# Kernel optimization log

Hardware: AMD Instinct MI355X
Metric: run time of the kernel (lower is better)

Reference implementation:

```python
import jax, jax.numpy as jnp
import numpy as np

B, N, D = 8, 2048, 16   # batch, n_points, n_dim (num_df == D)
K, DM = 32, 256         # k neighbors, d_model


def setup_inputs() -> dict:
    key = jax.random.key(0)
    k0, k1, k2, k3, k4, k5 = jax.random.split(key, 6)
    x = jax.random.normal(k0, (B, N, D), jnp.float32)
    features = jax.random.uniform(k1, (B, D), jnp.float32)
    # nn.Linear(k, d_model, bias=False) weights: [out, in] = [DM, K]
    lim = 1.0 / np.sqrt(K)
    W_crd = jax.random.uniform(k2, (DM, K), jnp.float32, -lim, lim)
    W_ftr = jax.random.uniform(k3, (DM, K), jnp.float32, -lim, lim)
    pe_crd = 0.01 * jax.random.normal(k4, (1, 1, D, DM), jnp.float32)
    pe_ftr = 0.01 * jax.random.normal(k5, (1, 1, D, DM), jnp.float32)
    return {"x": x, "features": features, "W_crd": W_crd, "W_ftr": W_ftr,
            "pe_crd": pe_crd, "pe_ftr": pe_ftr, "k": K}


def _forward(x, features, W_crd, W_ftr, pe_crd, pe_ftr, k):
    b, n, d = x.shape
    # split coordinates vs features per-dimension
    fmask = features[:, None, :] > 0.1                 # [B,1,D]
    x_crd = jnp.where(fmask, 0.0, x)                   # masked_fill(features_, 0)
    x_ftr = jnp.where(fmask, x, 0.0)                   # masked_fill(~features_, 0)
    xc = jnp.concatenate([x_crd, x_ftr], axis=-1)      # [B,N,2D]
    # masked stats with attn_mask=None -> plain mean / unbiased std over points
    mean = jnp.mean(xc, axis=1, keepdims=True)
    std = jnp.std(xc, axis=1, keepdims=True, ddof=1)
    xc = jnp.clip((xc - mean) / (std + 1e-5), -10.0, 10.0)
    # pairwise L2 distances on coordinate part (torch.cdist, p=2)
    sq = jnp.sum(x_crd * x_crd, axis=-1)               # [B,N]
    d2 = sq[:, :, None] + sq[:, None, :] - 2.0 * jnp.einsum('bnd,bmd->bnm', x_crd, x_crd)
    dist = jnp.sqrt(jnp.maximum(d2, 0.0))              # [B,N,N]
    # k nearest neighbors (smallest distance, self included)
    _, idx = jax.lax.top_k(-dist, k)                   # [B,N,k]
    nb = xc[jnp.arange(b)[:, None, None], idx]         # gather neighbors [B,N,k,2D]
    local = nb - xc[:, :, None, :]                     # project_local: center frame
    xk = jnp.transpose(local, (0, 1, 3, 2))            # flatten=False -> [B,N,2D,k]
    crd, ftr = xk[:, :, :d, :], xk[:, :, d:, :]
    o_crd = (jnp.einsum('bnpk,dk->bnpd', crd, W_crd) + pe_crd).sum(axis=2)
    o_ftr = (jnp.einsum('bnpk,dk->bnpd', ftr, W_ftr) + pe_ftr).sum(axis=2)
    pe_loss = jnp.abs(pe_crd).sum() + jnp.abs(pe_ftr).sum()
    # dropout is identity in eval mode
    return o_crd + o_ftr, pe_loss


def reference(x, features, W_crd, W_ftr, pe_crd, pe_ftr, k):
    return _forward(x, features, W_crd, W_ftr, pe_crd, pe_ftr, k)
```

## Files before the change

kernel.cpp:

```cpp
#include <hip/hip_runtime.h>
#include <stdint.h>

#define B 8
#define N 2048
#define D 16
#define KNN 32
#define DM 256
#define CAP 256

__global__ __launch_bounds__(256) void knn_prep(
    const float* __restrict__ x, const float* __restrict__ features,
    const float* __restrict__ Wc, const float* __restrict__ Wf,
    const float* __restrict__ pec, const float* __restrict__ pef,
    float* __restrict__ xcrdT, float* __restrict__ sq,
    float* __restrict__ Tc, float* __restrict__ Tf,
    float* __restrict__ WcT, float* __restrict__ WfT,
    float* __restrict__ cbias, float* __restrict__ pe_loss_out)
{
    if (blockIdx.x == 64) {
        int dm = threadIdx.x;
        float cb = 0.f, al = 0.f;
#pragma unroll
        for (int p = 0; p < D; ++p)
            cb += pec[p * DM + dm] + pef[p * DM + dm];
#pragma unroll
        for (int p = 0; p < D; ++p)
            al += fabsf(pec[p * DM + dm]) + fabsf(pef[p * DM + dm]);
        cbias[dm] = cb;
#pragma unroll
        for (int k = 0; k < KNN; ++k) {
            WcT[k * DM + dm] = Wc[dm * KNN + k];
            WfT[k * DM + dm] = Wf[dm * KNN + k];
        }
        __shared__ float redf[256];
        redf[dm] = al; __syncthreads();
        for (int st = 128; st > 0; st >>= 1) {
            if (dm < st) redf[dm] += redf[dm + st];
            __syncthreads();
        }
        if (dm == 0) pe_loss_out[0] = redf[0];
        return;
    }

    int tid = threadIdx.x;
    int b = blockIdx.x >> 3;

    double ls[D], lq[D];
#pragma unroll
    for (int d = 0; d < D; ++d) { ls[d] = 0.0; lq[d] = 0.0; }
    for (int r = 0; r < 8; ++r) {
        const float* row = x + ((size_t)b * N + r * 256 + tid) * D;
#pragma unroll
        for (int d = 0; d < D; d += 4) {
            float4 v = *(const float4*)(row + d);
            double x0 = v.x, x1 = v.y, x2 = v.z, x3 = v.w;
            ls[d]   += x0; lq[d]   += x0 * x0;
            ls[d+1] += x1; lq[d+1] += x1 * x1;
            ls[d+2] += x2; lq[d+2] += x2 * x2;
            ls[d+3] += x3; lq[d+3] += x3 * x3;
        }
    }
#pragma unroll
    for (int d = 0; d < D; ++d) {
        double s = ls[d], q = lq[d];
#pragma unroll
        for (int st = 32; st >= 1; st >>= 1) {
            s += __shfl_xor(s, st, 64);
            q += __shfl_xor(q, st, 64);
        }
        ls[d] = s; lq[d] = q;
    }
    __shared__ double sred[4][2 * D];
    __shared__ float smean[32], sscale[32];
    int wave = tid >> 6, lane = tid & 63;
    if (lane == 0) {
#pragma unroll
        for (int d = 0; d < D; ++d) {
            sred[wave][d]     = ls[d];
            sred[wave][D + d] = lq[d];
        }
    }
    __syncthreads();
    if (tid < D) {
        int d = tid;
        double S = sred[0][d] + sred[1][d] + sred[2][d] + sred[3][d];
        double Q = sred[0][D+d] + sred[1][D+d] + sred[2][D+d] + sred[3][D+d];
        double mean = S / (double)N;
        double var  = (Q - S * S / (double)N) / (double)(N - 1);
        if (var < 0.0) var = 0.0;
        float stdv = (float)sqrt(var);
        float scl  = 1.0f / (stdv + 1e-5f);
        float scl0 = 1.0f / (0.0f + 1e-5f);
        bool mask = features[b * D + d] > 0.1f;
        smean [d]      = mask ? 0.0f : (float)mean;
        sscale[d]      = mask ? scl0 : scl;
        smean [16 + d] = mask ? (float)mean : 0.0f;
        sscale[16 + d] = mask ? scl : scl0;
    }
    __syncthreads();

    int t = blockIdx.x * 256 + tid;
    int nn = t & (N - 1);
    float tc = 0.f, tf = 0.f, s = 0.f;
    float row[D];
#pragma unroll
    for (int d = 0; d < D; ++d) {
        float xv = x[(size_t)t * D + d];
        bool mask = features[b * D + d] > 0.1f;
        float xc = mask ? 0.f : xv;
        float xf = mask ? xv : 0.f;
        row[d] = xc;
        s += xc * xc;
        float vc = (xc - smean[d])      * sscale[d];
        vc = fminf(10.f, fmaxf(-10.f, vc));
        float vf = (xf - smean[16 + d]) * sscale[16 + d];
        vf = fminf(10.f, fmaxf(-10.f, vf));
        tc += vc; tf += vf;
    }
#pragma unroll
    for (int d = 0; d < D; ++d)
        xcrdT[((size_t)b * D + d) * N + nn] = row[d];
    sq[t] = s; Tc[t] = tc; Tf[t] = tf;
}

#define LOADBUF(buf, sqm, j) do {                                   \
    int m_ = (j) * 64 + lane;                                       \
    _Pragma("unroll")                                               \
    for (int d_ = 0; d_ < D; ++d_)                                  \
        buf[d_] = xbT[(size_t)d_ * N + m_];                         \
    sqm = sqb[m_];                                                  \
} while (0)

#define COMPUTE(j, buf, sqm) do {                                   \
    float dot0_ = 0.f, dot1_ = 0.f;                                 \
    _Pragma("unroll")                                               \
    for (int d_ = 0; d_ < D; ++d_) {                                \
        dot0_ += qx0[d_] * buf[d_];                                 \
        dot1_ += qx1[d_] * buf[d_];                                 \
    }                                                               \
    orig0[j] = fabsf(sqrtf(fmaxf(sqn0 + sqm - 2.0f * dot0_, 0.f))); \
    orig1[j] = fabsf(sqrtf(fmaxf(sqn1 + sqm - 2.0f * dot1_, 0.f))); \
} while (0)

__global__ __launch_bounds__(64, 2) void knn_main(
    const float* __restrict__ xcrdT, const float* __restrict__ sq,
    const float* __restrict__ Tc, const float* __restrict__ Tf,
    const float* __restrict__ WcT, const float* __restrict__ WfT,
    const float* __restrict__ cbias, float* __restrict__ out)
{
    __shared__ unsigned long long collect[2][CAP];
    __shared__ int sortedm[2][KNN];
    __shared__ float akbk[2][KNN][2];

    const int lane = threadIdx.x;
    const int qid0 = blockIdx.x * 2;
    const int b  = qid0 >> 11;
    const int n0 = qid0 & (N - 1);
    const int n1 = n0 + 1;

    const float* xbT = xcrdT + (size_t)b * D * N;
    const float* sqb = sq + b * N;

    float qx0[D], qx1[D];
#pragma unroll
    for (int d = 0; d < D; ++d) {
        float2 v = *(const float2*)(xbT + (size_t)d * N + n0);
        qx0[d] = v.x; qx1[d] = v.y;
    }
    const float sqn0 = sqb[n0], sqn1 = sqb[n1];

    float orig0[KNN], orig1[KNN];
    {
        float buf0[D], buf1[D];
        float sqm0v, sqm1v;
        LOADBUF(buf0, sqm0v, 0);
#pragma unroll
        for (int jj = 0; jj < KNN; jj += 2) {
            LOADBUF(buf1, sqm1v, jj + 1);
            COMPUTE(jj, buf0, sqm0v);
            if (jj + 2 < KNN) LOADBUF(buf0, sqm0v, jj + 2);
            COMPUTE(jj + 1, buf1, sqm1v);
        }
    }

    float v0 = orig0[0], v1 = orig1[0];
#pragma unroll
    for (int j = 1; j < KNN; ++j) {
        v0 = fminf(v0, orig0[j]);
        v1 = fminf(v1, orig1[j]);
    }
#pragma unroll
    for (int k = 2; k <= 64; k <<= 1) {
#pragma unroll
        for (int j = k >> 1; j >= 1; j >>= 1) {
            float o0 = __shfl_xor(v0, j, 64);
            float o1 = __shfl_xor(v1, j, 64);
            bool lower = (lane & j) == 0;
            bool up    = (lane & k) == 0;
            v0 = (lower == up) ? fminf(v0, o0) : fmaxf(v0, o0);
            v1 = (lower == up) ? fminf(v1, o1) : fmaxf(v1, o1);
        }
    }
    const float tau0 = __shfl(v0, 31, 64);
    const float tau1 = __shfl(v1, 31, 64);

    const unsigned long long lmask = (1ULL << lane) - 1ULL;
    int T0, T1;
    {
        int base = 0;
#pragma unroll
        for (int j = 0; j < KNN; ++j) {
            bool f = (orig0[j] <= tau0);
            unsigned long long mk = __ballot(f);
            if (f) {
                int pos = base + (int)__popcll(mk & lmask);
                if (pos < CAP)
                    collect[0][pos] =
                        (((unsigned long long)__float_as_uint(orig0[j])) << 11)
                        | (unsigned)(j * 64 + lane);
            }
            base += (int)__popcll(mk);
        }
        T0 = base < CAP ? base : CAP;
    }
    {
        int base = 0;
#pragma unroll
        for (int j = 0; j < KNN; ++j) {
            bool f = (orig1[j] <= tau1);
            unsigned long long mk = __ballot(f);
            if (f) {
                int pos = base + (int)__popcll(mk & lmask);
                if (pos < CAP)
                    collect[1][pos] =
                        (((unsigned long long)__float_as_uint(orig1[j])) << 11)
                        | (unsigned)(j * 64 + lane);
            }
            base += (int)__popcll(mk);
        }
        T1 = base < CAP ? base : CAP;
    }
    __syncthreads();

    if (T0 <= 64 && T1 <= 64) {
        unsigned long long key0 = (lane < T0) ? collect[0][lane] : ~0ULL;
        unsigned long long key1 = (lane < T1) ? collect[1][lane] : ~0ULL;
#pragma unroll
        for (int k = 2; k <= 64; k <<= 1) {
#pragma unroll
            for (int j = k >> 1; j >= 1; j >>= 1) {
                unsigned long long o0 = __shfl_xor(key0, j, 64);
                unsigned long long o1 = __shfl_xor(key1, j, 64);
                bool lower = (lane & j) == 0;
                bool up    = (lane & k) == 0;
                unsigned long long mn0 = (o0 < key0) ? o0 : key0;
                unsigned long long mx0 = (o0 < key0) ? key0 : o0;
                unsigned long long mn1 = (o1 < key1) ? o1 : key1;
                unsigned long long mx1 = (o1 < key1) ? key1 : o1;
                key0 = (lower == up) ? mn0 : mx0;
                key1 = (lower == up) ? mn1 : mx1;
            }
        }
        if (lane < KNN) {
            sortedm[0][lane] = (int)(key0 & 2047u);
            sortedm[1][lane] = (int)(key1 & 2047u);
        }
    } else {
#pragma unroll 1
        for (int q = 0; q < 2; ++q) {
            int T = q ? T1 : T0;
            unsigned long long* co = collect[q];
            int* so = sortedm[q];
            if (T <= 64) {
                unsigned long long key = (lane < T) ? co[lane] : ~0ULL;
#pragma unroll
                for (int k = 2; k <= 64; k <<= 1) {
#pragma unroll
                    for (int j = k >> 1; j >= 1; j >>= 1) {
                        unsigned long long o = __shfl_xor(key, j, 64);
                        bool lower = (lane & j) == 0;
                        bool up    = (lane & k) == 0;
                        unsigned long long mn = (o < key) ? o : key;
                        unsigned long long mx = (o < key) ? key : o;
                        key = (lower == up) ? mn : mx;
                    }
                }
                if (lane < KNN) so[lane] = (int)(key & 2047u);
            } else {
#pragma unroll 1
                for (int slot = 0; slot < CAP / 64; ++slot) {
                    int i = lane + slot * 64;
                    if (i < T) {
                        unsigned long long mk = co[i];
                        int rank = 0;
#pragma unroll 4
                        for (int t2 = 0; t2 < T; ++t2)
                            rank += (co[t2] < mk) ? 1 : 0;
                        if (rank < KNN) so[rank] = (int)(mk & 2047u);
                    }
                }
            }
        }
    }
    __syncthreads();

    const float* Tcb = Tc + b * N;
    const float* Tfb = Tf + b * N;
    {
        const float Tcn0 = Tcb[n0], Tfn0 = Tfb[n0];
        const float Tcn1 = Tcb[n1], Tfn1 = Tfb[n1];
        int q = lane >> 5;
        int k = lane & 31;
        int wm = sortedm[q][k];
        float av = Tcb[wm] - (q ? Tcn1 : Tcn0);
        float bv = Tfb[wm] - (q ? Tfn1 : Tfn0);
        akbk[q][k][0] = av;
        akbk[q][k][1] = bv;
    }
    __syncthreads();

    float acc0[4] = {0.f, 0.f, 0.f, 0.f};
    float acc1[4] = {0.f, 0.f, 0.f, 0.f};

#pragma unroll
    for (int k = 0; k < KNN; ++k) {
        float ak0 = akbk[0][k][0], bk0 = akbk[0][k][1];
        float ak1 = akbk[1][k][0], bk1 = akbk[1][k][1];
        const float* wc = WcT + k * DM + lane;
        const float* wf = WfT + k * DM + lane;
#pragma unroll
        for (int q = 0; q < 4; ++q) {
            float wcv = wc[q * 64];
            float wfv = wf[q * 64];
            acc0[q] += wcv * ak0 + wfv * bk0;
            acc1[q] += wcv * ak1 + wfv * bk1;
        }
    }

    size_t ob0 = (size_t)qid0 * DM + lane;
#pragma unroll
    for (int q = 0; q < 4; ++q) {
        float cb = cbias[lane + q * 64];
        out[ob0 + q * 64]      = acc0[q] + cb;
        out[ob0 + DM + q * 64] = acc1[q] + cb;
    }
}

extern "C" void kernel_launch(void* const* d_in, const int* in_sizes, int n_in,
                              void* d_out, int out_size, void* d_ws, size_t ws_size,
                              hipStream_t stream)
{
    const float* x        = (const float*)d_in[0];
    const float* features = (const float*)d_in[1];
    const float* W_crd    = (const float*)d_in[2];
    const float* W_ftr    = (const float*)d_in[3];
    const float* pe_crd   = (const float*)d_in[4];
    const float* pe_ftr   = (const float*)d_in[5];

    float* out = (float*)d_out;

    float* xcrdT = (float*)d_ws;
    float* sqv   = xcrdT + (size_t)B * N * D;
    float* Tc    = sqv  + B * N;
    float* Tf    = Tc   + B * N;
    float* cbias = Tf   + B * N;
    float* WcT   = cbias + DM;
    float* WfT   = WcT + KNN * DM;

    knn_prep<<<65, 256, 0, stream>>>(x, features, W_crd, W_ftr, pe_crd, pe_ftr,
                                     xcrdT, sqv, Tc, Tf, WcT, WfT, cbias,
                                     out + (size_t)out_size - 1);
    knn_main<<<(B * N) / 2, 64, 0, stream>>>(xcrdT, sqv, Tc, Tf,
                                             WcT, WfT, cbias, out);
}
```

Before: 177.9 us.

## Process four queries per wavefront in knn_main to reuse candidate loads

Each 64-lane block now handles four query points instead of two, so every candidate coordinate load is reused across four distance dot products, and the weight loads in the projection loop are shared by four outputs. The running minimum is folded into the distance loop instead of being taken in a separate pass. The cost is more registers (four 32-element distance arrays plus four query vectors), which may cause spills or lower occupancy under the launch-bounds hint, and the grid has half as many blocks.

```diff
diff --git a/kernel.cpp b/kernel.cpp
--- a/kernel.cpp
+++ b/kernel.cpp
@@ -131,15 +131,40 @@
     sqm = sqb[m_];                                                  \
 } while (0)
 
-#define COMPUTE(j, buf, sqm) do {                                   \
-    float dot0_ = 0.f, dot1_ = 0.f;                                 \
+#define COMPUTE4(j, buf, sqm) do {                                  \
+    float a0_ = 0.f, a1_ = 0.f, a2_ = 0.f, a3_ = 0.f;               \
     _Pragma("unroll")                                               \
     for (int d_ = 0; d_ < D; ++d_) {                                \
-        dot0_ += qx0[d_] * buf[d_];                                 \
-        dot1_ += qx1[d_] * buf[d_];                                 \
+        float v_ = buf[d_];                                         \
+        a0_ += qx0[d_] * v_;                                        \
+        a1_ += qx1[d_] * v_;                                        \
+        a2_ += qx2[d_] * v_;                                        \
+        a3_ += qx3[d_] * v_;                                        \
     }                                                               \
-    orig0[j] = fabsf(sqrtf(fmaxf(sqn0 + sqm - 2.0f * dot0_, 0.f))); \
-    orig1[j] = fabsf(sqrtf(fmaxf(sqn1 + sqm - 2.0f * dot1_, 0.f))); \
+    orig0[j] = fabsf(sqrtf(fmaxf(sqn0 + sqm - 2.0f * a0_, 0.f)));   \
+    orig1[j] = fabsf(sqrtf(fmaxf(sqn1 + sqm - 2.0f * a1_, 0.f)));   \
+    orig2[j] = fabsf(sqrtf(fmaxf(sqn2 + sqm - 2.0f * a2_, 0.f)));   \
+    orig3[j] = fabsf(sqrtf(fmaxf(sqn3 + sqm - 2.0f * a3_, 0.f)));   \
+    vm0 = fminf(vm0, orig0[j]); vm1 = fminf(vm1, orig1[j]);         \
+    vm2 = fminf(vm2, orig2[j]); vm3 = fminf(vm3, orig3[j]);         \
+} while (0)
+
+#define COMPACT(origX, tauX, cidx, TX) do {                         \
+    int base_ = 0;                                                  \
+    _Pragma("unroll")                                               \
+    for (int j_ = 0; j_ < KNN; ++j_) {                              \
+        bool f_ = (origX[j_] <= tauX);                              \
+        unsigned long long mk_ = __ballot(f_);                      \
+        if (f_) {                                                   \
+            int pos_ = base_ + (int)__popcll(mk_ & lmask);          \
+            if (pos_ < CAP)                                         \
+                collect[cidx][pos_] =                               \
+                    (((unsigned long long)__float_as_uint(origX[j_])) << 11) \
+                    | (unsigned)(j_ * 64 + lane);                   \
+        }                                                           \
+        base_ += (int)__popcll(mk_);                                \
+    }                                                               \
+    TX = base_ < CAP ? base_ : CAP;                                 \
 } while (0)
 
 __global__ __launch_bounds__(64, 2) void knn_main(
@@ -148,28 +173,30 @@
     const float* __restrict__ WcT, const float* __restrict__ WfT,
     const float* __restrict__ cbias, float* __restrict__ out)
 {
-    __shared__ unsigned long long collect[2][CAP];
-    __shared__ int sortedm[2][KNN];
-    __shared__ float akbk[2][KNN][2];
+    __shared__ unsigned long long collect[4][CAP];
+    __shared__ int sortedm[4][KNN];
+    __shared__ float akbk[4][KNN][2];
 
     const int lane = threadIdx.x;
-    const int qid0 = blockIdx.x * 2;
+    const int qid0 = blockIdx.x * 4;
     const int b  = qid0 >> 11;
     const int n0 = qid0 & (N - 1);
-    const int n1 = n0 + 1;
+    const int n1 = n0 + 1, n2 = n0 + 2, n3 = n0 + 3;
 
     const float* xbT = xcrdT + (size_t)b * D * N;
     const float* sqb = sq + b * N;
 
-    float qx0[D], qx1[D];
+    float qx0[D], qx1[D], qx2[D], qx3[D];
 #pragma unroll
     for (int d = 0; d < D; ++d) {
-        float2 v = *(const float2*)(xbT + (size_t)d * N + n0);
-        qx0[d] = v.x; qx1[d] = v.y;
+        float4 v = *(const float4*)(xbT + (size_t)d * N + n0);
+        qx0[d] = v.x; qx1[d] = v.y; qx2[d] = v.z; qx3[d] = v.w;
     }
     const float sqn0 = sqb[n0], sqn1 = sqb[n1];
-
-    float orig0[KNN], orig1[KNN];
+    const float sqn2 = sqb[n2], sqn3 = sqb[n3];
+
+    float orig0[KNN], orig1[KNN], orig2[KNN], orig3[KNN];
+    float vm0 = 1e30f, vm1 = 1e30f, vm2 = 1e30f, vm3 = 1e30f;
     {
         float buf0[D], buf1[D];
         float sqm0v, sqm1v;
@@ -177,98 +204,81 @@
 #pragma unroll
         for (int jj = 0; jj < KNN; jj += 2) {
             LOADBUF(buf1, sqm1v, jj + 1);
-            COMPUTE(jj, buf0, sqm0v);
+            COMPUTE4(jj, buf0, sqm0v);
             if (jj + 2 < KNN) LOADBUF(buf0, sqm0v, jj + 2);
-            COMPUTE(jj + 1, buf1, sqm1v);
-        }
-    }
-
-    float v0 = orig0[0], v1 = orig1[0];
-#pragma unroll
-    for (int j = 1; j < KNN; ++j) {
-        v0 = fminf(v0, orig0[j]);
-        v1 = fminf(v1, orig1[j]);
-    }
+            COMPUTE4(jj + 1, buf1, sqm1v);
+        }
+    }
+
 #pragma unroll
     for (int k = 2; k <= 64; k <<= 1) {
 #pragma unroll
         for (int j = k >> 1; j >= 1; j >>= 1) {
-            float o0 = __shfl_xor(v0, j, 64);
-            float o1 = __shfl_xor(v1, j, 64);
+            float o0 = __shfl_xor(vm0, j, 64);
+            float o1 = __shfl_xor(vm1, j, 64);
+            float o2 = __shfl_xor(vm2, j, 64);
+            float o3 = __shfl_xor(vm3, j, 64);
             bool lower = (lane & j) == 0;
             bool up    = (lane & k) == 0;
-            v0 = (lower == up) ? fminf(v0, o0) : fmaxf(v0, o0);
-            v1 = (lower == up) ? fminf(v1, o1) : fmaxf(v1, o1);
-        }
-    }
-    const float tau0 = __shfl(v0, 31, 64);
-    const float tau1 = __shfl(v1, 31, 64);
+            vm0 = (lower == up) ? fminf(vm0, o0) : fmaxf(vm0, o0);
+            vm1 = (lower == up) ? fminf(vm1, o1) : fmaxf(vm1, o1);
+            vm2 = (lower == up) ? fminf(vm2, o2) : fmaxf(vm2, o2);
+            vm3 = (lower == up) ? fminf(vm3, o3) : fmaxf(vm3, o3);
+        }
+    }
+    const float tau0 = __shfl(vm0, 31, 64);
+    const float tau1 = __shfl(vm1, 31, 64);
+    const float tau2 = __shfl(vm2, 31, 64);
+    const float tau3 = __shfl(vm3, 31, 64);
 
     const unsigned long long lmask = (1ULL << lane) - 1ULL;
-    int T0, T1;
-    {
-        int base = 0;
-#pragma unroll
-        for (int j = 0; j < KNN; ++j) {
-            bool f = (orig0[j] <= tau0);
-            unsigned long long mk = __ballot(f);
-            if (f) {
-                int pos = base + (int)__popcll(mk & lmask);
-                if (pos < CAP)
-                    collect[0][pos] =
-                        (((unsigned long long)__float_as_uint(orig0[j])) << 11)
-                        | (unsigned)(j * 64 + lane);
-            }
-            base += (int)__popcll(mk);
-        }
-        T0 = base < CAP ? base : CAP;
-    }
-    {
-        int base = 0;
-#pragma unroll
-        for (int j = 0; j < KNN; ++j) {
-            bool f = (orig1[j] <= tau1);
-            unsigned long long mk = __ballot(f);
-            if (f) {
-                int pos = base + (int)__popcll(mk & lmask);
-                if (pos < CAP)
-                    collect[1][pos] =
-                        (((unsigned long long)__float_as_uint(orig1[j])) << 11)
-                        | (unsigned)(j * 64 + lane);
-            }
-            base += (int)__popcll(mk);
-        }
-        T1 = base < CAP ? base : CAP;
-    }
+    int T0, T1, T2, T3;
+    COMPACT(orig0, tau0, 0, T0);
+    COMPACT(orig1, tau1, 1, T1);
+    COMPACT(orig2, tau2, 2, T2);
+    COMPACT(orig3, tau3, 3, T3);
     __syncthreads();
 
-    if (T0 <= 64 && T1 <= 64) {
+    if (T0 <= 64 && T1 <= 64 && T2 <= 64 && T3 <= 64) {
         unsigned long long key0 = (lane < T0) ? collect[0][lane] : ~0ULL;
         unsigned long long key1 = (lane < T1) ? collect[1][lane] : ~0ULL;
+        unsigned long long key2 = (lane < T2) ? collect[2][lane] : ~0ULL;
+        unsigned long long key3 = (lane < T3) ? collect[3][lane] : ~0ULL;
 #pragma unroll
         for (int k = 2; k <= 64; k <<= 1) {
 #pragma unroll
             for (int j = k >> 1; j >= 1; j >>= 1) {
                 unsigned long long o0 = __shfl_xor(key0, j, 64);
                 unsigned long long o1 = __shfl_xor(key1, j, 64);
+                unsigned long long o2 = __shfl_xor(key2, j, 64);
+                unsigned long long o3 = __shfl_xor(key3, j, 64);
                 bool lower = (lane & j) == 0;
                 bool up    = (lane & k) == 0;
+                bool sel   = (lower == up);
                 unsigned long long mn0 = (o0 < key0) ? o0 : key0;
                 unsigned long long mx0 = (o0 < key0) ? key0 : o0;
+                key0 = sel ? mn0 : mx0;
                 unsigned long long mn1 = (o1 < key1) ? o1 : key1;
                 unsigned long long mx1 = (o1 < key1) ? key1 : o1;
-                key0 = (lower == up) ? mn0 : mx0;
-                key1 = (lower == up) ? mn1 : mx1;
+                key1 = sel ? mn1 : mx1;
+                unsigned long long mn2 = (o2 < key2) ? o2 : key2;
+                unsigned long long mx2 = (o2 < key2) ? key2 : o2;
+                key2 = sel ? mn2 : mx2;
+                unsigned long long mn3 = (o3 < key3) ? o3 : key3;
+                unsigned long long mx3 = (o3 < key3) ? key3 : o3;
+                key3 = sel ? mn3 : mx3;
             }
         }
         if (lane < KNN) {
             sortedm[0][lane] = (int)(key0 & 2047u);
             sortedm[1][lane] = (int)(key1 & 2047u);
+            sortedm[2][lane] = (int)(key2 & 2047u);
+            sortedm[3][lane] = (int)(key3 & 2047u);
         }
     } else {
 #pragma unroll 1
-        for (int q = 0; q < 2; ++q) {
-            int T = q ? T1 : T0;
+        for (int q = 0; q < 4; ++q) {
+            int T = (q == 0) ? T0 : (q == 1) ? T1 : (q == 2) ? T2 : T3;
             unsigned long long* co = collect[q];
             int* so = sortedm[q];
             if (T <= 64) {
@@ -309,23 +319,34 @@
     {
         const float Tcn0 = Tcb[n0], Tfn0 = Tfb[n0];
         const float Tcn1 = Tcb[n1], Tfn1 = Tfb[n1];
-        int q = lane >> 5;
-        int k = lane & 31;
-        int wm = sortedm[q][k];
-        float av = Tcb[wm] - (q ? Tcn1 : Tcn0);
-        float bv = Tfb[wm] - (q ? Tfn1 : Tfn0);
-        akbk[q][k][0] = av;
-        akbk[q][k][1] = bv;
+        const float Tcn2 = Tcb[n2], Tfn2 = Tfb[n2];
+        const float Tcn3 = Tcb[n3], Tfn3 = Tfb[n3];
+        int k  = lane & 31;
+        int qh = lane >> 5;
+        int wmA = sortedm[qh][k];
+        float TcnA = qh ? Tcn1 : Tcn0;
+        float TfnA = qh ? Tfn1 : Tfn0;
+        akbk[qh][k][0] = Tcb[wmA] - TcnA;
+        akbk[qh][k][1] = Tfb[wmA] - TfnA;
+        int wmB = sortedm[2 + qh][k];
+        float TcnB = qh ? Tcn3 : Tcn2;
+        float TfnB = qh ? Tfn3 : Tfn2;
+        akbk[2 + qh][k][0] = Tcb[wmB] - TcnB;
+        akbk[2 + qh][k][1] = Tfb[wmB] - TfnB;
     }
     __syncthreads();
 
     float acc0[4] = {0.f, 0.f, 0.f, 0.f};
     float acc1[4] = {0.f, 0.f, 0.f, 0.f};
+    float acc2[4] = {0.f, 0.f, 0.f, 0.f};
+    float acc3[4] = {0.f, 0.f, 0.f, 0.f};
 
 #pragma unroll
     for (int k = 0; k < KNN; ++k) {
         float ak0 = akbk[0][k][0], bk0 = akbk[0][k][1];
         float ak1 = akbk[1][k][0], bk1 = akbk[1][k][1];
+        float ak2 = akbk[2][k][0], bk2 = akbk[2][k][1];
+        float ak3 = akbk[3][k][0], bk3 = akbk[3][k][1];
         const float* wc = WcT + k * DM + lane;
         const float* wf = WfT + k * DM + lane;
 #pragma unroll
@@ -334,6 +355,8 @@
             float wfv = wf[q * 64];
             acc0[q] += wcv * ak0 + wfv * bk0;
             acc1[q] += wcv * ak1 + wfv * bk1;
+            acc2[q] += wcv * ak2 + wfv * bk2;
+            acc3[q] += wcv * ak3 + wfv * bk3;
         }
     }
 
@@ -341,8 +364,10 @@
 #pragma unroll
     for (int q = 0; q < 4; ++q) {
         float cb = cbias[lane + q * 64];
-        out[ob0 + q * 64]      = acc0[q] + cb;
-        out[ob0 + DM + q * 64] = acc1[q] + cb;
+        out[ob0 + q * 64]          = acc0[q] + cb;
+        out[ob0 + DM + q * 64]     = acc1[q] + cb;
+        out[ob0 + 2 * DM + q * 64] = acc2[q] + cb;
+        out[ob0 + 3 * DM + q * 64] = acc3[q] + cb;
     }
 }
 
@@ -370,6 +395,6 @@
     knn_prep<<<65, 256, 0, stream>>>(x, features, W_crd, W_ftr, pe_crd, pe_ftr,
                                      xcrdT, sqv, Tc, Tf, WcT, WfT, cbias,
                                      out + (size_t)out_size - 1);
-    knn_main<<<(B * N) / 2, 64, 0, stream>>>(xcrdT, sqv, Tc, Tf,
+    knn_main<<<(B * N) / 4, 64, 0, stream>>>(xcrdT, sqv, Tc, Tf,
                                              WcT, WfT, cbias, out);
 }
```

After: 223.2 us. +25.5%, slower.
